# Optimization experiments

Hardware: AMD Instinct MI355X
Metric: run time of the kernel (lower is better)

Reference implementation:

```python
import jax, jax.numpy as jnp
import numpy as np

EMBED_DIM = 256
NUM_HEADS = 8
HEAD_DIM = EMBED_DIM // NUM_HEADS
SCALING = HEAD_DIM ** 0.5  # NOTE: module MULTIPLIES q by sqrt(head_dim), faithful to source


def setup_inputs() -> dict:
    key = jax.random.key(0)
    ks = jax.random.split(key, 10)
    B, S, D = 8, 1024, EMBED_DIM
    w = lambda k: jax.random.normal(k, (D, D), dtype=jnp.float32) * (1.0 / np.sqrt(D))
    b = lambda k: jax.random.normal(k, (D,), dtype=jnp.float32) * 0.01
    return {
        "hidden_states": jax.random.normal(ks[0], (B, S, D), dtype=jnp.float32),
        "object_queries": jax.random.normal(ks[1], (B, S, D), dtype=jnp.float32),
        "Wq": w(ks[2]), "bq": b(ks[3]),
        "Wk": w(ks[4]), "bk": b(ks[5]),
        "Wv": w(ks[6]), "bv": b(ks[7]),
        "Wo": w(ks[8]), "bo": b(ks[9]),
    }


def reference(hidden_states, object_queries, Wq, bq, Wk, bk, Wv, bv, Wo, bo):
    B, S, D = hidden_states.shape
    hs_pos = hidden_states + object_queries  # with_pos_embed for q and k
    # nn.Linear: x @ W.T + b (W is [out, in])
    q = (hs_pos @ Wq.T + bq) * SCALING
    k = hs_pos @ Wk.T + bk
    v = hidden_states @ Wv.T + bv  # value uses original hidden states (no pos)
    # [B, S, H, Dh]
    q = q.reshape(B, S, NUM_HEADS, HEAD_DIM)
    k = k.reshape(B, S, NUM_HEADS, HEAD_DIM)
    v = v.reshape(B, S, NUM_HEADS, HEAD_DIM)
    scores = jnp.einsum("bqhd,bkhd->bhqk", q, k)  # [B, H, S, S]
    probs = jax.nn.softmax(scores, axis=-1)
    out = jnp.einsum("bhqk,bkhd->bqhd", probs, v).reshape(B, S, D)
    return out @ Wo.T + bo
```

## Files before the change

kernel.cpp:

```cpp
#include <hip/hip_runtime.h>
#include <math.h>

#define BATCH 8
#define SEQ 1024
#define DM 256
#define NH 8
#define DH 32
#define MTOT (BATCH*SEQ)
#define LOG2E 1.4426950408889634f
#define SCALING 5.656854249492381f
#define QSCALE (SCALING * LOG2E)

typedef __attribute__((ext_vector_type(8))) short short8;
typedef __attribute__((ext_vector_type(4))) float f32x4;
typedef __attribute__((ext_vector_type(4))) unsigned short us4;
typedef _Float16 f16;
typedef __attribute__((ext_vector_type(8))) _Float16 f16x8;
typedef __attribute__((ext_vector_type(4))) _Float16 f16x4;

__device__ inline unsigned short f2bf(float f){
  union { float f; unsigned u; } x; x.f = f;
  unsigned r = x.u + 0x7fffu + ((x.u >> 16) & 1u);
  return (unsigned short)(r >> 16);
}
__device__ inline float bf2f(unsigned short s){
  union { unsigned u; float f; } x; x.u = ((unsigned)s) << 16;
  return x.f;
}
__device__ inline float fast_exp2(float x){
  float r; asm("v_exp_f32 %0, %1" : "=v"(r) : "v"(x)); return r;
}

__device__ inline f32x4 mfma_bf16(short8 a, short8 b, f32x4 c){
  return __builtin_amdgcn_mfma_f32_16x16x32_bf16(a, b, c, 0, 0, 0);
}
__device__ inline f32x4 mfma_f16_32(f16x8 a, f16x8 b, f32x4 c){
  return __builtin_amdgcn_mfma_f32_16x16x32_f16(a, b, c, 0, 0, 0);
}
__device__ inline f32x4 mfma_f16_16(f16x4 a, f16x4 b, f32x4 c){
  return __builtin_amdgcn_mfma_f32_16x16x16f16(a, b, c, 0, 0, 0);
}

__global__ __launch_bounds__(256) void prep_x_kernel(
    const float* __restrict__ hs, const float* __restrict__ oq,
    unsigned short* __restrict__ xph, unsigned short* __restrict__ xpl,
    f16* __restrict__ xv){
  const int n4 = MTOT * DM / 4;
  for (int i = blockIdx.x * blockDim.x + threadIdx.x; i < n4;
       i += gridDim.x * blockDim.x){
    f32x4 h = ((const f32x4*)hs)[i];
    f32x4 q = ((const f32x4*)oq)[i];
    us4 ph, pl; f16x4 xv4;
#pragma unroll
    for (int j = 0; j < 4; ++j){
      float p = h[j] + q[j];
      unsigned short hi = f2bf(p);
      ph[j] = hi;
      pl[j] = f2bf(p - bf2f(hi));
      xv4[j] = (f16)h[j];
    }
    ((us4*)xph)[i] = ph;
    ((us4*)xpl)[i] = pl;
    ((f16x4*)xv)[i] = xv4;
  }
}

__global__ __launch_bounds__(256) void prep_w_kernel(
    const float* __restrict__ Wq, const float* __restrict__ Wk,
    const float* __restrict__ Wv, const float* __restrict__ Wo,
    unsigned short* __restrict__ wqh, unsigned short* __restrict__ wql,
    unsigned short* __restrict__ wkh, unsigned short* __restrict__ wkl,
    f16* __restrict__ wv16, f16* __restrict__ wo16){
  int i = blockIdx.x * blockDim.x + threadIdx.x;
  if (i < DM * DM){
    float q = Wq[i];
    unsigned short qh_ = f2bf(q);
    wqh[i] = qh_; wql[i] = f2bf(q - bf2f(qh_));
    float k = Wk[i];
    unsigned short kh_ = f2bf(k);
    wkh[i] = kh_; wkl[i] = f2bf(k - bf2f(kh_));
    wv16[i] = (f16)Wv[i];
    wo16[i] = (f16)Wo[i];
  }
}

__global__ __launch_bounds__(256, 2) void proj_qkv_kernel(
    const unsigned short* __restrict__ xph, const unsigned short* __restrict__ xpl,
    const f16* __restrict__ xv,
    const unsigned short* __restrict__ wqh, const unsigned short* __restrict__ wql,
    const unsigned short* __restrict__ wkh, const unsigned short* __restrict__ wkl,
    const f16* __restrict__ wv16,
    const float* __restrict__ bq, const float* __restrict__ bk, const float* __restrict__ bv,
    unsigned short* __restrict__ qhp, unsigned short* __restrict__ qlp,
    unsigned short* __restrict__ khp, unsigned short* __restrict__ klp,
    f16* __restrict__ vT){
  __shared__ unsigned short XH[128][40];
  __shared__ unsigned short XL[128][40];
  __shared__ f16 XV[128][40];
  __shared__ unsigned short WQH[64][40];
  __shared__ unsigned short WQL[64][40];
  __shared__ unsigned short WKH[64][40];
  __shared__ unsigned short WKL[64][40];
  __shared__ f16 WV[64][40];
  __shared__ f16 VTT[64][144];
  const int tid = threadIdx.x;
  const int lane = tid & 63, wave = tid >> 6;
  const int bid = blockIdx.x;
  const int xcd = bid & 7, g = bid >> 3;
  const int nb = g & 3, mb = xcd * 8 + (g >> 2);
  const int m0 = mb * 128, n0 = nb * 64;
  const int wm = wave >> 1, wn = wave & 1;
  const int r = lane & 15, jj = lane >> 4;

  const int sr = tid >> 2, ssl = (tid & 3) * 8;
  const size_t xo0 = (size_t)(m0 + sr) * DM + ssl;
  const size_t xo1 = (size_t)(m0 + sr + 64) * DM + ssl;
  const size_t wo = (size_t)(n0 + sr) * DM + ssl;

  short8 rxh0, rxh1, rxl0, rxl1, rwq, rwql_, rwk, rwkl_;
  f16x8 rxv0, rxv1, rwv;
  rxh0 = *(const short8*)(xph + xo0); rxh1 = *(const short8*)(xph + xo1);
  rxl0 = *(const short8*)(xpl + xo0); rxl1 = *(const short8*)(xpl + xo1);
  rxv0 = *(const f16x8*)(xv + xo0);   rxv1 = *(const f16x8*)(xv + xo1);
  rwq = *(const short8*)(wqh + wo);   rwql_ = *(const short8*)(wql + wo);
  rwk = *(const short8*)(wkh + wo);   rwkl_ = *(const short8*)(wkl + wo);
  rwv = *(const f16x8*)(wv16 + wo);

  f32x4 aq[4][2], ak[4][2], av[4][2];
#pragma unroll
  for (int mi = 0; mi < 4; ++mi)
#pragma unroll
    for (int ni = 0; ni < 2; ++ni){
      aq[mi][ni] = (f32x4){0.f,0.f,0.f,0.f};
      ak[mi][ni] = (f32x4){0.f,0.f,0.f,0.f};
      av[mi][ni] = (f32x4){0.f,0.f,0.f,0.f};
    }

  for (int kk = 0; kk < DM; kk += 32){
    __syncthreads();
    *(short8*)&XH[sr][ssl] = rxh0;  *(short8*)&XH[sr + 64][ssl] = rxh1;
    *(short8*)&XL[sr][ssl] = rxl0;  *(short8*)&XL[sr + 64][ssl] = rxl1;
    *(f16x8*)&XV[sr][ssl] = rxv0;   *(f16x8*)&XV[sr + 64][ssl] = rxv1;
    *(short8*)&WQH[sr][ssl] = rwq;  *(short8*)&WQL[sr][ssl] = rwql_;
    *(short8*)&WKH[sr][ssl] = rwk;  *(short8*)&WKL[sr][ssl] = rwkl_;
    *(f16x8*)&WV[sr][ssl] = rwv;
    __syncthreads();
    if (kk + 32 < DM){
      const int o = kk + 32;
      rxh0 = *(const short8*)(xph + xo0 + o); rxh1 = *(const short8*)(xph + xo1 + o);
      rxl0 = *(const short8*)(xpl + xo0 + o); rxl1 = *(const short8*)(xpl + xo1 + o);
      rxv0 = *(const f16x8*)(xv + xo0 + o);   rxv1 = *(const f16x8*)(xv + xo1 + o);
      rwq = *(const short8*)(wqh + wo + o);   rwql_ = *(const short8*)(wql + wo + o);
      rwk = *(const short8*)(wkh + wo + o);   rwkl_ = *(const short8*)(wkl + wo + o);
      rwv = *(const f16x8*)(wv16 + wo + o);
    }
#pragma unroll
    for (int ni = 0; ni < 2; ++ni){
      const int brow = wn * 32 + ni * 16 + r;
      short8 bwqh = *(const short8*)&WQH[brow][jj * 8];
      short8 bwql = *(const short8*)&WQL[brow][jj * 8];
      short8 bwkh = *(const short8*)&WKH[brow][jj * 8];
      short8 bwkl = *(const short8*)&WKL[brow][jj * 8];
      f16x8 bwv = *(const f16x8*)&WV[brow][jj * 8];
#pragma unroll
      for (int mi = 0; mi < 4; ++mi){
        const int arow = wm * 64 + mi * 16 + r;
        short8 axh = *(const short8*)&XH[arow][jj * 8];
        short8 axl = *(const short8*)&XL[arow][jj * 8];
        f16x8 axv = *(const f16x8*)&XV[arow][jj * 8];
        aq[mi][ni] = mfma_bf16(axh, bwqh, aq[mi][ni]);
        aq[mi][ni] = mfma_bf16(axh, bwql, aq[mi][ni]);
        aq[mi][ni] = mfma_bf16(axl, bwqh, aq[mi][ni]);
        ak[mi][ni] = mfma_bf16(axh, bwkh, ak[mi][ni]);
        ak[mi][ni] = mfma_bf16(axh, bwkl, ak[mi][ni]);
        ak[mi][ni] = mfma_bf16(axl, bwkh, ak[mi][ni]);
        av[mi][ni] = mfma_f16_32(axv, bwv, av[mi][ni]);
      }
    }
  }
#pragma unroll
  for (int ni = 0; ni < 2; ++ni){
    const int col = n0 + wn * 32 + ni * 16 + r;
    const float bqc = bq[col] * QSCALE;
    const float bkc = bk[col];
    const float bvc = bv[col];
#pragma unroll
    for (int mi = 0; mi < 4; ++mi){
      f16x4 v4;
#pragma unroll
      for (int rr = 0; rr < 4; ++rr){
        const int row = m0 + wm * 64 + mi * 16 + jj * 4 + rr;
        float qv = aq[mi][ni][rr] * QSCALE + bqc;
        unsigned short qhi = f2bf(qv);
        qhp[row * DM + col] = qhi;
        qlp[row * DM + col] = f2bf(qv - bf2f(qhi));
        float kv = ak[mi][ni][rr] + bkc;
        unsigned short khi = f2bf(kv);
        khp[row * DM + col] = khi;
        klp[row * DM + col] = f2bf(kv - bf2f(khi));
        v4[rr] = (f16)(av[mi][ni][rr] + bvc);
      }
      *(f16x4*)&VTT[wn * 32 + ni * 16 + r][wm * 64 + mi * 16 + jj * 4] = v4;
    }
  }
  __syncthreads();
  const int batch = m0 >> 10;
  const int s0 = m0 & 1023;
  const int c = tid >> 2, sblk = (tid & 3) * 32;
  f16* dst = vT + ((size_t)(batch * DM + n0 + c)) * SEQ + s0 + sblk;
#pragma unroll
  for (int u = 0; u < 4; ++u){
    *(f16x8*)(dst + u * 8) = *(const f16x8*)&VTT[c][sblk + u * 8];
  }
}

__global__ __launch_bounds__(256) void attn_kernel(
    const unsigned short* __restrict__ qh, const unsigned short* __restrict__ ql,
    const unsigned short* __restrict__ kh, const unsigned short* __restrict__ kl,
    const f16* __restrict__ vT, f16* __restrict__ aout){
  __shared__ unsigned short KH[2][64][40];
  __shared__ unsigned short KL[2][64][40];
  __shared__ f16 VT[2][32][72];
  const int lane = threadIdx.x & 63;
  const int wave = threadIdx.x >> 6;
  const int tid = threadIdx.x;
  const int xcd = blockIdx.x & 7, j = blockIdx.x >> 3;
  const int bh = xcd * 8 + (j & 7);
  const int qb = j >> 3;
  const int b = bh >> 3, h = bh & 7;
  const int q0 = (qb * 4 + wave) * 32;
  const int rowbase = b * SEQ;
  const int col0 = h * DH;
  const int r = lane & 15, jj = lane >> 4;

  const int qrowA = rowbase + q0 + r;
  const int qrowB = qrowA + 16;
  short8 bqhA = *(const short8*)(qh + qrowA * DM + col0 + jj * 8);
  short8 bqlA = *(const short8*)(ql + qrowA * DM + col0 + jj * 8);
  short8 bqhB = *(const short8*)(qh + qrowB * DM + col0 + jj * 8);
  short8 bqlB = *(const short8*)(ql + qrowB * DM + col0 + jj * 8);

  const int skey = tid >> 2, ssl = tid & 3;
  const unsigned short* khsrc = kh + (size_t)(rowbase + skey) * DM + col0 + ssl * 8;
  const unsigned short* klsrc = kl + (size_t)(rowbase + skey) * DM + col0 + ssl * 8;
  const int sdh = tid >> 3, ss8 = tid & 7;
  const f16* vsrc = vT + (size_t)(b * DM + col0 + sdh) * SEQ + ss8 * 8;

  short8 rkh = *(const short8*)(khsrc);
  short8 rkl = *(const short8*)(klsrc);
  f16x8 rv = *(const f16x8*)(vsrc);

  float mA = -INFINITY, lsumA = 0.f;
  float mB = -INFINITY, lsumB = 0.f;
  f32x4 o0a = {0.f,0.f,0.f,0.f}, o1a = {0.f,0.f,0.f,0.f};
  f32x4 o0b = {0.f,0.f,0.f,0.f}, o1b = {0.f,0.f,0.f,0.f};

  for (int c = 0; c < SEQ; c += 64){
    const int p = (c >> 6) & 1;
    *(short8*)&KH[p][skey][ssl * 8] = rkh;
    *(short8*)&KL[p][skey][ssl * 8] = rkl;
    *(f16x8*)&VT[p][sdh][ss8 * 8] = rv;
    __syncthreads();
    if (c + 64 < SEQ){
      rkh = *(const short8*)(khsrc + (size_t)(c + 64) * DM);
      rkl = *(const short8*)(klsrc + (size_t)(c + 64) * DM);
      rv = *(const f16x8*)(vsrc + c + 64);
    }
    f32x4 sA[4], sB[4];
    float cmaxA = -INFINITY, cmaxB = -INFINITY;
#pragma unroll
    for (int t = 0; t < 4; ++t){
      short8 akh = *(const short8*)&KH[p][t * 16 + r][jj * 8];
      short8 akl = *(const short8*)&KL[p][t * 16 + r][jj * 8];
      f32x4 sv = {0.f,0.f,0.f,0.f};
      sv = mfma_bf16(akh, bqhA, sv);
      sv = mfma_bf16(akh, bqlA, sv);
      sv = mfma_bf16(akl, bqhA, sv);
      sA[t] = sv;
      cmaxA = fmaxf(cmaxA, fmaxf(fmaxf(sv[0], sv[1]), fmaxf(sv[2], sv[3])));
      f32x4 sw = {0.f,0.f,0.f,0.f};
      sw = mfma_bf16(akh, bqhB, sw);
      sw = mfma_bf16(akh, bqlB, sw);
      sw = mfma_bf16(akl, bqhB, sw);
      sB[t] = sw;
      cmaxB = fmaxf(cmaxB, fmaxf(fmaxf(sw[0], sw[1]), fmaxf(sw[2], sw[3])));
    }
    cmaxA = fmaxf(cmaxA, __shfl_xor(cmaxA, 16, 64));
    cmaxA = fmaxf(cmaxA, __shfl_xor(cmaxA, 32, 64));
    cmaxB = fmaxf(cmaxB, __shfl_xor(cmaxB, 16, 64));
    cmaxB = fmaxf(cmaxB, __shfl_xor(cmaxB, 32, 64));
    if (!__all(cmaxA - mA <= 8.0f)){
      const float mnew = fmaxf(mA, cmaxA);
      const float scale = fast_exp2(mA - mnew);
      lsumA *= scale;
#pragma unroll
      for (int rr = 0; rr < 4; ++rr){ o0a[rr] *= scale; o1a[rr] *= scale; }
      mA = mnew;
    }
    if (!__all(cmaxB - mB <= 8.0f)){
      const float mnew = fmaxf(mB, cmaxB);
      const float scale = fast_exp2(mB - mnew);
      lsumB *= scale;
#pragma unroll
      for (int rr = 0; rr < 4; ++rr){ o0b[rr] *= scale; o1b[rr] *= scale; }
      mB = mnew;
    }
    float psA = 0.f, psB = 0.f;
    f16x4 bpA[4], bpB[4];
#pragma unroll
    for (int t = 0; t < 4; ++t){
      float a0 = fast_exp2(sA[t][0] - mA);
      float a1 = fast_exp2(sA[t][1] - mA);
      float a2 = fast_exp2(sA[t][2] - mA);
      float a3 = fast_exp2(sA[t][3] - mA);
      psA += (a0 + a1) + (a2 + a3);
      f16x4 ba; ba[0]=(f16)a0; ba[1]=(f16)a1; ba[2]=(f16)a2; ba[3]=(f16)a3;
      bpA[t] = ba;
      float b0 = fast_exp2(sB[t][0] - mB);
      float b1 = fast_exp2(sB[t][1] - mB);
      float b2 = fast_exp2(sB[t][2] - mB);
      float b3 = fast_exp2(sB[t][3] - mB);
      psB += (b0 + b1) + (b2 + b3);
      f16x4 bb; bb[0]=(f16)b0; bb[1]=(f16)b1; bb[2]=(f16)b2; bb[3]=(f16)b3;
      bpB[t] = bb;
    }
    psA += __shfl_xor(psA, 16, 64);
    psA += __shfl_xor(psA, 32, 64);
    lsumA += psA;
    psB += __shfl_xor(psB, 16, 64);
    psB += __shfl_xor(psB, 32, 64);
    lsumB += psB;
#pragma unroll
    for (int t = 0; t < 4; ++t){
      f16x4 av0 = *(const f16x4*)&VT[p][r][t * 16 + jj * 4];
      f16x4 av1 = *(const f16x4*)&VT[p][16 + r][t * 16 + jj * 4];
      o0a = mfma_f16_16(av0, bpA[t], o0a);
      o1a = mfma_f16_16(av1, bpA[t], o1a);
      o0b = mfma_f16_16(av0, bpB[t], o0b);
      o1b = mfma_f16_16(av1, bpB[t], o1b);
    }
  }
  const float invA = 1.f / lsumA;
  const float invB = 1.f / lsumB;
  const int orowA = qrowA * DM + col0;
  const int orowB = qrowB * DM + col0;
#pragma unroll
  for (int rr = 0; rr < 4; ++rr){
    const int dh = jj * 4 + rr;
    aout[orowA + dh] = (f16)(o0a[rr] * invA);
    aout[orowA + 16 + dh] = (f16)(o1a[rr] * invA);
    aout[orowB + dh] = (f16)(o0b[rr] * invB);
    aout[orowB + 16 + dh] = (f16)(o1b[rr] * invB);
  }
}

__global__ __launch_bounds__(256, 4) void oproj_kernel(
    const f16* __restrict__ attn, const f16* __restrict__ wo16,
    const float* __restrict__ bo, float* __restrict__ out){
  __shared__ f16 AT[128][40];
  __shared__ f16 WO[64][40];
  const int tid = threadIdx.x;
  const int lane = tid & 63, wave = tid >> 6;
  const int bid = blockIdx.x;
  const int xcd = bid & 7, g = bid >> 3;
  const int nb = g & 3, mb = xcd * 8 + (g >> 2);
  const int m0 = mb * 128, n0 = nb * 64;
  const int wm = wave >> 1, wn = wave & 1;
  const int r = lane & 15, jj = lane >> 4;
  const int sr = tid >> 2, ssl = (tid & 3) * 8;
  const f16* asrc0 = attn + (size_t)(m0 + sr) * DM + ssl;
  const f16* asrc1 = attn + (size_t)(m0 + sr + 64) * DM + ssl;
  const f16* wsrc = wo16 + (size_t)(n0 + sr) * DM + ssl;
  f16x8 ra0 = *(const f16x8*)(asrc0);
  f16x8 ra1 = *(const f16x8*)(asrc1);
  f16x8 rw = *(const f16x8*)(wsrc);
  f32x4 acc[4][2];
#pragma unroll
  for (int mi = 0; mi < 4; ++mi){
    acc[mi][0] = (f32x4){0.f,0.f,0.f,0.f};
    acc[mi][1] = (f32x4){0.f,0.f,0.f,0.f};
  }
  for (int kk = 0; kk < DM; kk += 32){
    __syncthreads();
    *(f16x8*)&AT[sr][ssl] = ra0;
    *(f16x8*)&AT[sr + 64][ssl] = ra1;
    *(f16x8*)&WO[sr][ssl] = rw;
    __syncthreads();
    if (kk + 32 < DM){
      ra0 = *(const f16x8*)(asrc0 + kk + 32);
      ra1 = *(const f16x8*)(asrc1 + kk + 32);
      rw = *(const f16x8*)(wsrc + kk + 32);
    }
    f16x8 bf0 = *(const f16x8*)&WO[wn * 32 + r][jj * 8];
    f16x8 bf1 = *(const f16x8*)&WO[wn * 32 + 16 + r][jj * 8];
#pragma unroll
    for (int mi = 0; mi < 4; ++mi){
      f16x8 af = *(const f16x8*)&AT[wm * 64 + mi * 16 + r][jj * 8];
      acc[mi][0] = mfma_f16_32(af, bf0, acc[mi][0]);
      acc[mi][1] = mfma_f16_32(af, bf1, acc[mi][1]);
    }
  }
#pragma unroll
  for (int ni = 0; ni < 2; ++ni){
    const int col = n0 + wn * 32 + ni * 16 + r;
    const float bc = bo[col];
#pragma unroll
    for (int mi = 0; mi < 4; ++mi){
#pragma unroll
      for (int rr = 0; rr < 4; ++rr){
        const int row = m0 + wm * 64 + mi * 16 + jj * 4 + rr;
        out[row * DM + col] = acc[mi][ni][rr] + bc;
      }
    }
  }
}

extern "C" void kernel_launch(void* const* d_in, const int* in_sizes, int n_in,
                              void* d_out, int out_size, void* d_ws, size_t ws_size,
                              hipStream_t stream){
  const float* hs = (const float*)d_in[0];
  const float* oq = (const float*)d_in[1];
  const float* Wq = (const float*)d_in[2];
  const float* bq = (const float*)d_in[3];
  const float* Wk = (const float*)d_in[4];
  const float* bk = (const float*)d_in[5];
  const float* Wv = (const float*)d_in[6];
  const float* bv = (const float*)d_in[7];
  const float* Wo = (const float*)d_in[8];
  const float* bo = (const float*)d_in[9];
  float* out = (float*)d_out;

  char* p = (char*)d_ws;
  auto alloc = [&](size_t bytes) -> char* {
    char* r = p;
    p += (bytes + 255) & ~((size_t)255);
    return r;
  };
  const size_t xb = (size_t)MTOT * DM * 2;
  unsigned short* xph = (unsigned short*)alloc(xb);
  unsigned short* xpl = (unsigned short*)alloc(xb);
  f16* xv = (f16*)alloc(xb);
  unsigned short* qh = (unsigned short*)alloc(xb);
  unsigned short* ql = (unsigned short*)alloc(xb);
  unsigned short* kh = (unsigned short*)alloc(xb);
  unsigned short* kl = (unsigned short*)alloc(xb);
  f16* vT = (f16*)alloc(xb);
  f16* attn = (f16*)alloc(xb);
  const size_t wb = (size_t)DM * DM * 2;
  unsigned short* wqh = (unsigned short*)alloc(wb);
  unsigned short* wql = (unsigned short*)alloc(wb);
  unsigned short* wkh = (unsigned short*)alloc(wb);
  unsigned short* wkl = (unsigned short*)alloc(wb);
  f16* wv16 = (f16*)alloc(wb);
  f16* wo16 = (f16*)alloc(wb);

  hipLaunchKernelGGL(prep_x_kernel, dim3(1024), dim3(256), 0, stream,
                     hs, oq, xph, xpl, xv);
  hipLaunchKernelGGL(prep_w_kernel, dim3(DM * DM / 256), dim3(256), 0, stream,
                     Wq, Wk, Wv, Wo, wqh, wql, wkh, wkl, wv16, wo16);
  hipLaunchKernelGGL(proj_qkv_kernel, dim3(256), dim3(256), 0, stream,
                     xph, xpl, xv, wqh, wql, wkh, wkl, wv16, bq, bk, bv,
                     qh, ql, kh, kl, vT);
  hipLaunchKernelGGL(attn_kernel, dim3(512), dim3(256), 0, stream,
                     qh, ql, kh, kl, vT, attn);
  hipLaunchKernelGGL(oproj_kernel, dim3(256), dim3(256), 0, stream,
                     attn, wo16, bo, out);
}
```

Baseline: 69.20 us.

## Fuse input prep into QKV projection, split attention over keys, shrink oproj tiles

The separate prep_x pass is removed, and the QKV projection now reads fp32 inputs directly and converts them to bf16 hi/lo and fp16 in registers using packed convert instructions. Attention is split into two key halves (split-K, flash-decoding style) to double the grid. Each half writes scaled fp16 partial outputs plus max/sum, and a new merge kernel combines them. The output projection uses 64-row tiles, giving twice as many blocks. These changes aim to cut an HBM round trip and raise occupancy, but add a merge pass, partial-buffer traffic and fp16 rescaling risk.

```diff
diff --git a/kernel.cpp b/kernel.cpp
--- a/kernel.cpp
+++ b/kernel.cpp
@@ -10,10 +10,11 @@
 #define LOG2E 1.4426950408889634f
 #define SCALING 5.656854249492381f
 #define QSCALE (SCALING * LOG2E)
+#define NROW 65536
+#define OSC 0.0625f
 
 typedef __attribute__((ext_vector_type(8))) short short8;
 typedef __attribute__((ext_vector_type(4))) float f32x4;
-typedef __attribute__((ext_vector_type(4))) unsigned short us4;
 typedef _Float16 f16;
 typedef __attribute__((ext_vector_type(8))) _Float16 f16x8;
 typedef __attribute__((ext_vector_type(4))) _Float16 f16x4;
@@ -27,6 +28,14 @@
   union { unsigned u; float f; } x; x.u = ((unsigned)s) << 16;
   return x.f;
 }
+__device__ inline float u2f(unsigned u){
+  union { unsigned u; float f; } x; x.u = u; return x.f;
+}
+__device__ inline unsigned cvtpk_bf16(float a, float b){
+  unsigned r;
+  asm("v_cvt_pk_bf16_f32 %0, %1, %2" : "=v"(r) : "v"(a), "v"(b));
+  return r;
+}
 __device__ inline float fast_exp2(float x){
   float r; asm("v_exp_f32 %0, %1" : "=v"(r) : "v"(x)); return r;
 }
@@ -39,30 +48,6 @@
 }
 __device__ inline f32x4 mfma_f16_16(f16x4 a, f16x4 b, f32x4 c){
   return __builtin_amdgcn_mfma_f32_16x16x16f16(a, b, c, 0, 0, 0);
-}
-
-__global__ __launch_bounds__(256) void prep_x_kernel(
-    const float* __restrict__ hs, const float* __restrict__ oq,
-    unsigned short* __restrict__ xph, unsigned short* __restrict__ xpl,
-    f16* __restrict__ xv){
-  const int n4 = MTOT * DM / 4;
-  for (int i = blockIdx.x * blockDim.x + threadIdx.x; i < n4;
-       i += gridDim.x * blockDim.x){
-    f32x4 h = ((const f32x4*)hs)[i];
-    f32x4 q = ((const f32x4*)oq)[i];
-    us4 ph, pl; f16x4 xv4;
-#pragma unroll
-    for (int j = 0; j < 4; ++j){
-      float p = h[j] + q[j];
-      unsigned short hi = f2bf(p);
-      ph[j] = hi;
-      pl[j] = f2bf(p - bf2f(hi));
-      xv4[j] = (f16)h[j];
-    }
-    ((us4*)xph)[i] = ph;
-    ((us4*)xpl)[i] = pl;
-    ((f16x4*)xv)[i] = xv4;
-  }
 }
 
 __global__ __launch_bounds__(256) void prep_w_kernel(
@@ -85,8 +70,7 @@
 }
 
 __global__ __launch_bounds__(256, 2) void proj_qkv_kernel(
-    const unsigned short* __restrict__ xph, const unsigned short* __restrict__ xpl,
-    const f16* __restrict__ xv,
+    const float* __restrict__ hs, const float* __restrict__ oq,
     const unsigned short* __restrict__ wqh, const unsigned short* __restrict__ wql,
     const unsigned short* __restrict__ wkh, const unsigned short* __restrict__ wkl,
     const f16* __restrict__ wv16,
@@ -113,15 +97,40 @@
   const int r = lane & 15, jj = lane >> 4;
 
   const int sr = tid >> 2, ssl = (tid & 3) * 8;
-  const size_t xo0 = (size_t)(m0 + sr) * DM + ssl;
-  const size_t xo1 = (size_t)(m0 + sr + 64) * DM + ssl;
+  const float* hs0 = hs + (size_t)(m0 + sr) * DM + ssl;
+  const float* hs1 = hs0 + 64 * DM;
+  const float* oq0 = oq + (size_t)(m0 + sr) * DM + ssl;
+  const float* oq1 = oq0 + 64 * DM;
   const size_t wo = (size_t)(n0 + sr) * DM + ssl;
 
-  short8 rxh0, rxh1, rxl0, rxl1, rwq, rwql_, rwk, rwkl_;
-  f16x8 rxv0, rxv1, rwv;
-  rxh0 = *(const short8*)(xph + xo0); rxh1 = *(const short8*)(xph + xo1);
-  rxl0 = *(const short8*)(xpl + xo0); rxl1 = *(const short8*)(xpl + xo1);
-  rxv0 = *(const f16x8*)(xv + xo0);   rxv1 = *(const f16x8*)(xv + xo1);
+  auto convrow = [&](const float* hp, const float* op, int kk,
+                     short8& xh, short8& xl, f16x8& xv){
+    f32x4 ha = *(const f32x4*)(hp + kk);
+    f32x4 hb = *(const f32x4*)(hp + kk + 4);
+    f32x4 oa = *(const f32x4*)(op + kk);
+    f32x4 ob = *(const f32x4*)(op + kk + 4);
+    float p0 = ha[0]+oa[0], p1 = ha[1]+oa[1], p2 = ha[2]+oa[2], p3 = ha[3]+oa[3];
+    float p4 = hb[0]+ob[0], p5 = hb[1]+ob[1], p6 = hb[2]+ob[2], p7 = hb[3]+ob[3];
+    union { unsigned u[4]; short8 s; } H, L;
+    H.u[0] = cvtpk_bf16(p0, p1); H.u[1] = cvtpk_bf16(p2, p3);
+    H.u[2] = cvtpk_bf16(p4, p5); H.u[3] = cvtpk_bf16(p6, p7);
+    float l0 = p0 - u2f(H.u[0] << 16), l1 = p1 - u2f(H.u[0] & 0xffff0000u);
+    float l2 = p2 - u2f(H.u[1] << 16), l3 = p3 - u2f(H.u[1] & 0xffff0000u);
+    float l4 = p4 - u2f(H.u[2] << 16), l5 = p5 - u2f(H.u[2] & 0xffff0000u);
+    float l6 = p6 - u2f(H.u[3] << 16), l7 = p7 - u2f(H.u[3] & 0xffff0000u);
+    L.u[0] = cvtpk_bf16(l0, l1); L.u[1] = cvtpk_bf16(l2, l3);
+    L.u[2] = cvtpk_bf16(l4, l5); L.u[3] = cvtpk_bf16(l6, l7);
+    xh = H.s; xl = L.s;
+    f16x8 v;
+    v[0]=(f16)ha[0]; v[1]=(f16)ha[1]; v[2]=(f16)ha[2]; v[3]=(f16)ha[3];
+    v[4]=(f16)hb[0]; v[5]=(f16)hb[1]; v[6]=(f16)hb[2]; v[7]=(f16)hb[3];
+    xv = v;
+  };
+
+  short8 sxh0, sxh1, sxl0, sxl1, rwq, rwql_, rwk, rwkl_;
+  f16x8 sxv0, sxv1, rwv;
+  convrow(hs0, oq0, 0, sxh0, sxl0, sxv0);
+  convrow(hs1, oq1, 0, sxh1, sxl1, sxv1);
   rwq = *(const short8*)(wqh + wo);   rwql_ = *(const short8*)(wql + wo);
   rwk = *(const short8*)(wkh + wo);   rwkl_ = *(const short8*)(wkl + wo);
   rwv = *(const f16x8*)(wv16 + wo);
@@ -138,18 +147,17 @@
 
   for (int kk = 0; kk < DM; kk += 32){
     __syncthreads();
-    *(short8*)&XH[sr][ssl] = rxh0;  *(short8*)&XH[sr + 64][ssl] = rxh1;
-    *(short8*)&XL[sr][ssl] = rxl0;  *(short8*)&XL[sr + 64][ssl] = rxl1;
-    *(f16x8*)&XV[sr][ssl] = rxv0;   *(f16x8*)&XV[sr + 64][ssl] = rxv1;
+    *(short8*)&XH[sr][ssl] = sxh0;  *(short8*)&XH[sr + 64][ssl] = sxh1;
+    *(short8*)&XL[sr][ssl] = sxl0;  *(short8*)&XL[sr + 64][ssl] = sxl1;
+    *(f16x8*)&XV[sr][ssl] = sxv0;   *(f16x8*)&XV[sr + 64][ssl] = sxv1;
     *(short8*)&WQH[sr][ssl] = rwq;  *(short8*)&WQL[sr][ssl] = rwql_;
     *(short8*)&WKH[sr][ssl] = rwk;  *(short8*)&WKL[sr][ssl] = rwkl_;
     *(f16x8*)&WV[sr][ssl] = rwv;
     __syncthreads();
     if (kk + 32 < DM){
       const int o = kk + 32;
-      rxh0 = *(const short8*)(xph + xo0 + o); rxh1 = *(const short8*)(xph + xo1 + o);
-      rxl0 = *(const short8*)(xpl + xo0 + o); rxl1 = *(const short8*)(xpl + xo1 + o);
-      rxv0 = *(const f16x8*)(xv + xo0 + o);   rxv1 = *(const f16x8*)(xv + xo1 + o);
+      convrow(hs0, oq0, o, sxh0, sxl0, sxv0);
+      convrow(hs1, oq1, o, sxh1, sxl1, sxv1);
       rwq = *(const short8*)(wqh + wo + o);   rwql_ = *(const short8*)(wql + wo + o);
       rwk = *(const short8*)(wkh + wo + o);   rwkl_ = *(const short8*)(wkl + wo + o);
       rwv = *(const f16x8*)(wv16 + wo + o);
@@ -214,10 +222,10 @@
   }
 }
 
-__global__ __launch_bounds__(256) void attn_kernel(
+__global__ __launch_bounds__(256, 3) void attn_kernel(
     const unsigned short* __restrict__ qh, const unsigned short* __restrict__ ql,
     const unsigned short* __restrict__ kh, const unsigned short* __restrict__ kl,
-    const f16* __restrict__ vT, f16* __restrict__ aout){
+    const f16* __restrict__ vT, f16* __restrict__ opart, float* __restrict__ mlpart){
   __shared__ unsigned short KH[2][64][40];
   __shared__ unsigned short KL[2][64][40];
   __shared__ f16 VT[2][32][72];
@@ -226,10 +234,12 @@
   const int tid = threadIdx.x;
   const int xcd = blockIdx.x & 7, j = blockIdx.x >> 3;
   const int bh = xcd * 8 + (j & 7);
-  const int qb = j >> 3;
+  const int u = j >> 3;
+  const int qb = u & 7, half = u >> 3;
   const int b = bh >> 3, h = bh & 7;
   const int q0 = (qb * 4 + wave) * 32;
   const int rowbase = b * SEQ;
+  const int kbase = rowbase + half * 512;
   const int col0 = h * DH;
   const int r = lane & 15, jj = lane >> 4;
 
@@ -241,10 +251,10 @@
   short8 bqlB = *(const short8*)(ql + qrowB * DM + col0 + jj * 8);
 
   const int skey = tid >> 2, ssl = tid & 3;
-  const unsigned short* khsrc = kh + (size_t)(rowbase + skey) * DM + col0 + ssl * 8;
-  const unsigned short* klsrc = kl + (size_t)(rowbase + skey) * DM + col0 + ssl * 8;
+  const unsigned short* khsrc = kh + (size_t)(kbase + skey) * DM + col0 + ssl * 8;
+  const unsigned short* klsrc = kl + (size_t)(kbase + skey) * DM + col0 + ssl * 8;
   const int sdh = tid >> 3, ss8 = tid & 7;
-  const f16* vsrc = vT + (size_t)(b * DM + col0 + sdh) * SEQ + ss8 * 8;
+  const f16* vsrc = vT + (size_t)(b * DM + col0 + sdh) * SEQ + half * 512 + ss8 * 8;
 
   short8 rkh = *(const short8*)(khsrc);
   short8 rkl = *(const short8*)(klsrc);
@@ -255,13 +265,13 @@
   f32x4 o0a = {0.f,0.f,0.f,0.f}, o1a = {0.f,0.f,0.f,0.f};
   f32x4 o0b = {0.f,0.f,0.f,0.f}, o1b = {0.f,0.f,0.f,0.f};
 
-  for (int c = 0; c < SEQ; c += 64){
+  for (int c = 0; c < 512; c += 64){
     const int p = (c >> 6) & 1;
     *(short8*)&KH[p][skey][ssl * 8] = rkh;
     *(short8*)&KL[p][skey][ssl * 8] = rkl;
     *(f16x8*)&VT[p][sdh][ss8 * 8] = rv;
     __syncthreads();
-    if (c + 64 < SEQ){
+    if (c + 64 < 512){
       rkh = *(const short8*)(khsrc + (size_t)(c + 64) * DM);
       rkl = *(const short8*)(klsrc + (size_t)(c + 64) * DM);
       rv = *(const f16x8*)(vsrc + c + 64);
@@ -340,62 +350,85 @@
       o1b = mfma_f16_16(av1, bpB[t], o1b);
     }
   }
-  const float invA = 1.f / lsumA;
-  const float invB = 1.f / lsumB;
-  const int orowA = qrowA * DM + col0;
-  const int orowB = qrowB * DM + col0;
+  const size_t prowA = (size_t)(half * NROW + bh * 1024 + q0 + r);
+  const size_t prowB = prowA + 16;
+  f16x4 w0a, w1a, w0b, w1b;
 #pragma unroll
   for (int rr = 0; rr < 4; ++rr){
-    const int dh = jj * 4 + rr;
-    aout[orowA + dh] = (f16)(o0a[rr] * invA);
-    aout[orowA + 16 + dh] = (f16)(o1a[rr] * invA);
-    aout[orowB + dh] = (f16)(o0b[rr] * invB);
-    aout[orowB + 16 + dh] = (f16)(o1b[rr] * invB);
-  }
+    w0a[rr] = (f16)(o0a[rr] * OSC); w1a[rr] = (f16)(o1a[rr] * OSC);
+    w0b[rr] = (f16)(o0b[rr] * OSC); w1b[rr] = (f16)(o1b[rr] * OSC);
+  }
+  *(f16x4*)(opart + prowA * 32 + jj * 4) = w0a;
+  *(f16x4*)(opart + prowA * 32 + 16 + jj * 4) = w1a;
+  *(f16x4*)(opart + prowB * 32 + jj * 4) = w0b;
+  *(f16x4*)(opart + prowB * 32 + 16 + jj * 4) = w1b;
+  if (jj == 0){
+    ((float2*)mlpart)[prowA] = make_float2(mA, lsumA * OSC);
+    ((float2*)mlpart)[prowB] = make_float2(mB, lsumB * OSC);
+  }
+}
+
+__global__ __launch_bounds__(256) void merge_kernel(
+    const f16* __restrict__ opart, const float* __restrict__ mlpart,
+    f16* __restrict__ aout){
+  const int e = blockIdx.x * 256 + threadIdx.x;
+  const int dh4 = (e & 7) * 4;
+  const int row = e >> 3;
+  const int bh = row >> 10, qlr = row & 1023;
+  const int b = bh >> 3, h = bh & 7;
+  const float2 ml1 = ((const float2*)mlpart)[row];
+  const float2 ml2 = ((const float2*)mlpart)[NROW + row];
+  const float M = fmaxf(ml1.x, ml2.x);
+  const float s1 = fast_exp2(ml1.x - M);
+  const float s2 = fast_exp2(ml2.x - M);
+  const float inv = 1.f / (ml1.y * s1 + ml2.y * s2);
+  f16x4 o1 = *(const f16x4*)(opart + (size_t)row * 32 + dh4);
+  f16x4 o2 = *(const f16x4*)(opart + ((size_t)NROW + row) * 32 + dh4);
+  f16x4 o;
+#pragma unroll
+  for (int jji = 0; jji < 4; ++jji)
+    o[jji] = (f16)(((float)o1[jji] * s1 + (float)o2[jji] * s2) * inv);
+  *(f16x4*)(aout + ((size_t)(b * SEQ + qlr)) * DM + h * 32 + dh4) = o;
 }
 
 __global__ __launch_bounds__(256, 4) void oproj_kernel(
     const f16* __restrict__ attn, const f16* __restrict__ wo16,
     const float* __restrict__ bo, float* __restrict__ out){
-  __shared__ f16 AT[128][40];
+  __shared__ f16 AT[64][40];
   __shared__ f16 WO[64][40];
   const int tid = threadIdx.x;
   const int lane = tid & 63, wave = tid >> 6;
   const int bid = blockIdx.x;
   const int xcd = bid & 7, g = bid >> 3;
-  const int nb = g & 3, mb = xcd * 8 + (g >> 2);
-  const int m0 = mb * 128, n0 = nb * 64;
+  const int nb = g & 3, mb = xcd * 16 + (g >> 2);
+  const int m0 = mb * 64, n0 = nb * 64;
   const int wm = wave >> 1, wn = wave & 1;
   const int r = lane & 15, jj = lane >> 4;
   const int sr = tid >> 2, ssl = (tid & 3) * 8;
-  const f16* asrc0 = attn + (size_t)(m0 + sr) * DM + ssl;
-  const f16* asrc1 = attn + (size_t)(m0 + sr + 64) * DM + ssl;
+  const f16* asrc = attn + (size_t)(m0 + sr) * DM + ssl;
   const f16* wsrc = wo16 + (size_t)(n0 + sr) * DM + ssl;
-  f16x8 ra0 = *(const f16x8*)(asrc0);
-  f16x8 ra1 = *(const f16x8*)(asrc1);
+  f16x8 ra = *(const f16x8*)(asrc);
   f16x8 rw = *(const f16x8*)(wsrc);
-  f32x4 acc[4][2];
-#pragma unroll
-  for (int mi = 0; mi < 4; ++mi){
+  f32x4 acc[2][2];
+#pragma unroll
+  for (int mi = 0; mi < 2; ++mi){
     acc[mi][0] = (f32x4){0.f,0.f,0.f,0.f};
     acc[mi][1] = (f32x4){0.f,0.f,0.f,0.f};
   }
   for (int kk = 0; kk < DM; kk += 32){
     __syncthreads();
-    *(f16x8*)&AT[sr][ssl] = ra0;
-    *(f16x8*)&AT[sr + 64][ssl] = ra1;
+    *(f16x8*)&AT[sr][ssl] = ra;
     *(f16x8*)&WO[sr][ssl] = rw;
     __syncthreads();
     if (kk + 32 < DM){
-      ra0 = *(const f16x8*)(asrc0 + kk + 32);
-      ra1 = *(const f16x8*)(asrc1 + kk + 32);
+      ra = *(const f16x8*)(asrc + kk + 32);
       rw = *(const f16x8*)(wsrc + kk + 32);
     }
     f16x8 bf0 = *(const f16x8*)&WO[wn * 32 + r][jj * 8];
     f16x8 bf1 = *(const f16x8*)&WO[wn * 32 + 16 + r][jj * 8];
 #pragma unroll
-    for (int mi = 0; mi < 4; ++mi){
-      f16x8 af = *(const f16x8*)&AT[wm * 64 + mi * 16 + r][jj * 8];
+    for (int mi = 0; mi < 2; ++mi){
+      f16x8 af = *(const f16x8*)&AT[wm * 32 + mi * 16 + r][jj * 8];
       acc[mi][0] = mfma_f16_32(af, bf0, acc[mi][0]);
       acc[mi][1] = mfma_f16_32(af, bf1, acc[mi][1]);
     }
@@ -405,10 +438,10 @@
     const int col = n0 + wn * 32 + ni * 16 + r;
     const float bc = bo[col];
 #pragma unroll
-    for (int mi = 0; mi < 4; ++mi){
+    for (int mi = 0; mi < 2; ++mi){
 #pragma unroll
       for (int rr = 0; rr < 4; ++rr){
-        const int row = m0 + wm * 64 + mi * 16 + jj * 4 + rr;
+        const int row = m0 + wm * 32 + mi * 16 + jj * 4 + rr;
         out[row * DM + col] = acc[mi][ni][rr] + bc;
       }
     }
@@ -437,9 +470,6 @@
     return r;
   };
   const size_t xb = (size_t)MTOT * DM * 2;
-  unsigned short* xph = (unsigned short*)alloc(xb);
-  unsigned short* xpl = (unsigned short*)alloc(xb);
-  f16* xv = (f16*)alloc(xb);
   unsigned short* qh = (unsigned short*)alloc(xb);
   unsigned short* ql = (unsigned short*)alloc(xb);
   unsigned short* kh = (unsigned short*)alloc(xb);
@@ -453,16 +483,18 @@
   unsigned short* wkl = (unsigned short*)alloc(wb);
   f16* wv16 = (f16*)alloc(wb);
   f16* wo16 = (f16*)alloc(wb);
-
-  hipLaunchKernelGGL(prep_x_kernel, dim3(1024), dim3(256), 0, stream,
-                     hs, oq, xph, xpl, xv);
+  f16* opart = (f16*)alloc((size_t)2 * NROW * 32 * 2);
+  float* mlpart = (float*)alloc((size_t)2 * NROW * 2 * 4);
+
   hipLaunchKernelGGL(prep_w_kernel, dim3(DM * DM / 256), dim3(256), 0, stream,
                      Wq, Wk, Wv, Wo, wqh, wql, wkh, wkl, wv16, wo16);
   hipLaunchKernelGGL(proj_qkv_kernel, dim3(256), dim3(256), 0, stream,
-                     xph, xpl, xv, wqh, wql, wkh, wkl, wv16, bq, bk, bv,
+                     hs, oq, wqh, wql, wkh, wkl, wv16, bq, bk, bv,
                      qh, ql, kh, kl, vT);
-  hipLaunchKernelGGL(attn_kernel, dim3(512), dim3(256), 0, stream,
-                     qh, ql, kh, kl, vT, attn);
-  hipLaunchKernelGGL(oproj_kernel, dim3(256), dim3(256), 0, stream,
+  hipLaunchKernelGGL(attn_kernel, dim3(1024), dim3(256), 0, stream,
+                     qh, ql, kh, kl, vT, opart, mlpart);
+  hipLaunchKernelGGL(merge_kernel, dim3(2048), dim3(256), 0, stream,
+                     opart, mlpart, attn);
+  hipLaunchKernelGGL(oproj_kernel, dim3(512), dim3(256), 0, stream,
                      attn, wo16, bo, out);
 }
```

Result: faster. 67.24 us (-2.8%).
